# Kernel tuning notes

Measured on AMD Instinct MI355X. Metric: run time of the kernel, lower is better.

Reference implementation:

```python
import jax, jax.numpy as jnp
import numpy as np
from jax import lax

NB, HH, WW, C = 8, 64, 64, 192
G, K, DW_K, PA_K = 12, 3, 5, 3
GC, P = C // G, K * K
PAD, STRIDE, DIL = 1, 1, 1
OFFSET_SCALE = 1.0
LN_EPS = 1e-5


def _grid_sample(img, grid):
    # img: (B,Cc,H,W); grid: (B,L,P,2) xy in [-1,1]; bilinear, zeros padding, align_corners=False
    B, Cc, H, W = img.shape
    gx = (grid[..., 0] + 1.0) * (W * 0.5) - 0.5
    gy = (grid[..., 1] + 1.0) * (H * 0.5) - 0.5
    x0, y0 = jnp.floor(gx), jnp.floor(gy)

    def gather(xi, yi):
        valid = (xi >= 0) & (xi <= W - 1) & (yi >= 0) & (yi <= H - 1)
        xc = jnp.clip(xi, 0, W - 1).astype(jnp.int32)
        yc = jnp.clip(yi, 0, H - 1).astype(jnp.int32)
        v = jax.vmap(lambda im, y, x: im[:, y, x])(img, yc, xc)  # (B,Cc,L,P)
        return v * valid[:, None].astype(img.dtype)

    wx1, wy1 = gx - x0, gy - y0
    wx0, wy0 = 1.0 - wx1, 1.0 - wy1
    return (gather(x0, y0) * (wx0 * wy0)[:, None]
            + gather(x0 + 1.0, y0) * (wx1 * wy0)[:, None]
            + gather(x0, y0 + 1.0) * (wx0 * wy1)[:, None]
            + gather(x0 + 1.0, y0 + 1.0) * (wx1 * wy1)[:, None])


def _dcnv3_core(x, offset, mask):
    # x: (N,H,W,C) projected input; offset: (N,H,W,G*P*2); mask: (N,H,W,G*P)
    N, H, W, _ = x.shape
    xp = jnp.pad(x, ((0, 0), (PAD, PAD), (PAD, PAD), (0, 0)))
    Hp, Wp = H + 2 * PAD, W + 2 * PAD
    Ho, Wo = offset.shape[1], offset.shape[2]
    base = (DIL * (K - 1)) // 2 + 0.5
    ref_y = (base + jnp.arange(Ho) * STRIDE) / Hp
    ref_x = (base + jnp.arange(Wo) * STRIDE) / Wp
    ref = jnp.stack(jnp.broadcast_arrays(ref_x[None, :], ref_y[:, None]), -1)  # (Ho,Wo,2) xy
    start = -((DIL * (K - 1)) // 2)
    pts = (start + jnp.arange(K) * DIL).astype(x.dtype)
    gxg = jnp.broadcast_to((pts / Wp)[:, None], (K, K))  # w offset varies along dim0 (torch order)
    gyg = jnp.broadcast_to((pts / Hp)[None, :], (K, K))
    grid = jnp.tile(jnp.stack([gxg, gyg], -1).reshape(P, 2), (G, 1))  # (G*P,2)
    loc = ref[None, :, :, None, :] + grid * OFFSET_SCALE  # (1,Ho,Wo,G*P,2)
    norm = jnp.array([Wp, Hp], dtype=x.dtype)
    loc = loc + offset.reshape(N, Ho, Wo, G * P, 2) * OFFSET_SCALE / norm
    sg = 2.0 * loc - 1.0  # (N,Ho,Wo,G*P,2)
    img = xp.reshape(N, Hp * Wp, G, GC).transpose(0, 2, 3, 1).reshape(N * G, GC, Hp, Wp)
    grd = sg.reshape(N, Ho * Wo, G, P, 2).transpose(0, 2, 1, 3, 4).reshape(N * G, Ho * Wo, P, 2)
    samp = _grid_sample(img, grd)  # (N*G, GC, L, P)
    m = mask.reshape(N, Ho * Wo, G, P).transpose(0, 2, 1, 3).reshape(N * G, 1, Ho * Wo, P)
    out = (samp * m).sum(-1)  # (N*G, GC, L)
    return out.reshape(N, G, GC, Ho * Wo).transpose(0, 3, 1, 2).reshape(N, Ho, Wo, C)


def _dcnv3(x, dw_w, dw_b, ln_g, ln_b, off_w, off_b, msk_w, msk_b, in_w, in_b, out_w, out_b, cfs_w, cfs_b):
    N, H, W, _ = x.shape
    x_proj = x @ in_w + in_b
    # depthwise conv (5x5) -> LayerNorm (channels_last) -> GELU(exact)
    u = lax.conv_general_dilated(x, dw_w, (1, 1), 'SAME',
                                 dimension_numbers=('NHWC', 'HWIO', 'NHWC'),
                                 feature_group_count=C) + dw_b
    mu = u.mean(-1, keepdims=True)
    var = ((u - mu) ** 2).mean(-1, keepdims=True)
    u = (u - mu) * lax.rsqrt(var + LN_EPS) * ln_g + ln_b
    u = jax.nn.gelu(u, approximate=False)
    offset = u @ off_w + off_b  # (N,H,W,G*P*2)
    m = jax.nn.softmax((u @ msk_w + msk_b).reshape(N, H, W, G, P), axis=-1).reshape(N, H, W, G * P)
    y = _dcnv3_core(x_proj, offset, m)
    cfs = jax.nn.sigmoid(u @ cfs_w + cfs_b)  # (N,H,W,G)
    cfs = jnp.repeat(cfs, GC, axis=-1)       # (N,H,W,C), group-blockwise
    y = y * (1.0 - cfs) + x_proj * cfs
    return y @ out_w + out_b


def _patch_attention(x):
    # x: (N,H,W,C) -> std over softmax'd 3x3 neighbor scores: (N,H,W)
    N, H, W, _ = x.shape
    pad = (PA_K - 1) // 2
    xp = jnp.pad(x, ((0, 0), (pad, pad), (pad, pad), (0, 0)))
    neigh = jnp.stack([xp[:, i:i + H, j:j + W, :] for i in range(PA_K) for j in range(PA_K)],
                      axis=-1)  # (N,H,W,C,K1*K2), torch unfold ordering
    scores = jnp.einsum('nhwc,nhwck->nhwk', x, neigh)
    sm = jax.nn.softmax(scores, axis=-1)
    return jnp.std(sm, axis=-1, ddof=1)  # torch.std is unbiased


def setup_inputs() -> dict:
    key = jax.random.key(0)
    ks = jax.random.split(key, 8)
    s = 0.02
    return {
        'x': jax.random.normal(ks[0], (NB, HH, WW, C), jnp.float32),
        'dw_w': jax.random.normal(ks[1], (DW_K, DW_K, 1, C), jnp.float32) * s,
        'dw_b': jnp.zeros((C,), jnp.float32),
        'ln_g': jnp.ones((C,), jnp.float32),
        'ln_b': jnp.zeros((C,), jnp.float32),
        'off_w': jax.random.normal(ks[2], (C, G * P * 2), jnp.float32) * s,
        'off_b': jnp.zeros((G * P * 2,), jnp.float32),
        'msk_w': jax.random.normal(ks[3], (C, G * P), jnp.float32) * s,
        'msk_b': jnp.zeros((G * P,), jnp.float32),
        'in_w': jax.random.normal(ks[4], (C, C), jnp.float32) * s,
        'in_b': jnp.zeros((C,), jnp.float32),
        'out_w': jax.random.normal(ks[5], (C, C), jnp.float32) * s,
        'out_b': jnp.zeros((C,), jnp.float32),
        'cfs_w': jax.random.normal(ks[6], (C, G), jnp.float32) * s,
        'cfs_b': jnp.zeros((G,), jnp.float32),
    }


def reference(x, dw_w, dw_b, ln_g, ln_b, off_w, off_b, msk_w, msk_b, in_w, in_b, out_w, out_b, cfs_w, cfs_b):
    x1 = _dcnv3(x, dw_w, dw_b, ln_g, ln_b, off_w, off_b, msk_w, msk_b, in_w, in_b, out_w, out_b, cfs_w, cfs_b)
    mask = _patch_attention(x1)           # (N,H,W)
    return x + x1 * mask[..., None]
```

## Files before the change

### kernel.cpp

```cpp
#include <hip/hip_runtime.h>
#include <hip/hip_bf16.h>
#include <math.h>

#define NB 8
#define HH 64
#define WW 64
#define C 192
#define G 12
#define GC 16
#define P 9
#define NPIX (NB*HH*WW)

typedef __attribute__((ext_vector_type(8))) short short8;
typedef __attribute__((ext_vector_type(4))) float f32x4;
typedef unsigned short ushort;

__device__ __forceinline__ ushort to_bf16(float f) {
  __hip_bfloat16 b = __float2bfloat16(f);
  return *(ushort*)&b;
}
__device__ __forceinline__ float bf2f(ushort u) {
  union { unsigned u; float f; } cv; cv.u = ((unsigned)u) << 16; return cv.f;
}
__device__ __forceinline__ float bflo(unsigned u) {
  union { unsigned v; float f; } c; c.v = u << 16; return c.f;
}
__device__ __forceinline__ float bfhi(unsigned u) {
  union { unsigned v; float f; } c; c.v = u & 0xffff0000u; return c.f;
}

__global__ void prep_w_kernel(const float* __restrict__ in_w, const float* __restrict__ out_w,
    const float* __restrict__ off_w, const float* __restrict__ msk_w, const float* __restrict__ cfs_w,
    const float* __restrict__ off_b, const float* __restrict__ msk_b, const float* __restrict__ cfs_b,
    ushort* __restrict__ in_wt, ushort* __restrict__ out_wt, ushort* __restrict__ wf_t,
    float* __restrict__ bf_bias) {
  int idx = blockIdx.x*256 + threadIdx.x;
  if (idx < 36864) {
    int n = idx/192, k = idx%192;
    in_wt[idx] = to_bf16(in_w[k*192 + n]);
  } else if (idx < 73728) {
    int j = idx - 36864; int n = j/192, k = j%192;
    out_wt[j] = to_bf16(out_w[k*192 + n]);
  } else if (idx < 147456) {
    int j = idx - 73728; int n = j/192, k = j%192;
    float v = 0.f;
    if (n < 216)      v = off_w[k*216 + n];
    else if (n < 324) v = msk_w[k*108 + (n-216)];
    else if (n < 336) v = cfs_w[k*12  + (n-324)];
    wf_t[j] = to_bf16(v);
  }
  if (idx < 384) {
    float b = 0.f;
    if (idx < 216)      b = off_b[idx];
    else if (idx < 324) b = msk_b[idx-216];
    else if (idx < 336) b = cfs_b[idx-324];
    bf_bias[idx] = b;
  }
}

template<int NW, int NSTORE, bool BF16OUT, bool AF32>
__global__ __launch_bounds__(256) void mfma_gemm(const void* __restrict__ A_,
    const ushort* __restrict__ Wt, const float* __restrict__ bias,
    void* __restrict__ Cout_) {
  __shared__ ushort As[4*64*8];
  __shared__ ushort Bs[4*64*8];
  int pix0 = blockIdx.x * 64, n0 = blockIdx.y * 64;
  int tid = threadIdx.x;
  int wid = tid >> 6, lane = tid & 63;
  int wr = wid >> 1, wc = wid & 1;
  int lr = lane >> 4, lc = lane & 15;

  f32x4 acc[2][2];
  #pragma unroll
  for (int m=0;m<2;m++)
    #pragma unroll
    for (int j=0;j<2;j++) acc[m][j] = (f32x4){0.f,0.f,0.f,0.f};

  int s_kb = tid >> 6, s_row = tid & 63;

  short8 pa, pb;
  auto load_tile = [&](int k0) {
    if (AF32) {
      const float* Af = (const float*)A_;
      float4 u0 = *(const float4*)&Af[(size_t)(pix0 + s_row)*192 + k0 + s_kb*8];
      float4 u1 = *(const float4*)&Af[(size_t)(pix0 + s_row)*192 + k0 + s_kb*8 + 4];
      pa[0]=to_bf16(u0.x); pa[1]=to_bf16(u0.y); pa[2]=to_bf16(u0.z); pa[3]=to_bf16(u0.w);
      pa[4]=to_bf16(u1.x); pa[5]=to_bf16(u1.y); pa[6]=to_bf16(u1.z); pa[7]=to_bf16(u1.w);
    } else {
      const ushort* Ab = (const ushort*)A_;
      pa = *(const short8*)&Ab[(size_t)(pix0 + s_row)*192 + k0 + s_kb*8];
    }
    pb = *(const short8*)&Wt[(size_t)(n0 + s_row)*192 + k0 + s_kb*8];
  };
  load_tile(0);

  for (int t = 0; t < 6; t++) {
    __syncthreads();
    *(short8*)&As[(size_t)tid*8] = pa;
    *(short8*)&Bs[(size_t)tid*8] = pb;
    __syncthreads();
    if (t < 5) load_tile((t+1)*32);
    short8 a0 = *(const short8*)&As[(size_t)(lr*64 + wr*32 + lc)*8];
    short8 a1 = *(const short8*)&As[(size_t)(lr*64 + wr*32 + 16 + lc)*8];
    short8 b0 = *(const short8*)&Bs[(size_t)(lr*64 + wc*32 + lc)*8];
    short8 b1 = *(const short8*)&Bs[(size_t)(lr*64 + wc*32 + 16 + lc)*8];
    acc[0][0] = __builtin_amdgcn_mfma_f32_16x16x32_bf16(a0, b0, acc[0][0], 0,0,0);
    acc[0][1] = __builtin_amdgcn_mfma_f32_16x16x32_bf16(a0, b1, acc[0][1], 0,0,0);
    acc[1][0] = __builtin_amdgcn_mfma_f32_16x16x32_bf16(a1, b0, acc[1][0], 0,0,0);
    acc[1][1] = __builtin_amdgcn_mfma_f32_16x16x32_bf16(a1, b1, acc[1][1], 0,0,0);
  }
  #pragma unroll
  for (int j=0;j<2;j++) {
    int col = n0 + wc*32 + j*16 + lc;
    if (NW != NSTORE && col >= NSTORE) continue;
    float bb = bias[col];
    #pragma unroll
    for (int m=0;m<2;m++) {
      size_t rbase = pix0 + wr*32 + m*16 + lr*4;
      #pragma unroll
      for (int r=0;r<4;r++) {
        float v = acc[m][j][r] + bb;
        if (BF16OUT) ((ushort*)Cout_)[(rbase + r)*NSTORE + col] = to_bf16(v);
        else         ((float*) Cout_)[(rbase + r)*NSTORE + col] = v;
      }
    }
  }
}

#define SEG 16
__global__ __launch_bounds__(192) void dw_ln_gelu_kernel(const float* __restrict__ x,
    const float* __restrict__ dw_w, const float* __restrict__ dw_b,
    const float* __restrict__ ln_g, const float* __restrict__ ln_b,
    ushort* __restrict__ u_out) {
  int bid = blockIdx.x;
  int blk = (bid & 7) * 256 + (bid >> 3);
  int qw = blk & 3; int nh = blk >> 2;
  int h = nh & 63, n = nh >> 6;
  int c = threadIdx.x;
  int w0 = qw * SEG;

  float kw[25];
  #pragma unroll
  for (int t=0;t<25;t++) kw[t] = dw_w[t*C + c];

  float acc[SEG];
  float bb = dw_b[c];
  #pragma unroll
  for (int i=0;i<SEG;i++) acc[i] = bb;

  #pragma unroll
  for (int i=0;i<5;i++) {
    int hy = h + i - 2;
    if (hy < 0 || hy >= HH) continue;
    const float* rowp = &x[(((size_t)n*HH + hy)*WW)*C + c];
    #pragma unroll
    for (int wi=0; wi<SEG+4; wi++) {
      int w_in = w0 - 2 + wi;
      if (w_in < 0 || w_in >= WW) continue;
      float v = rowp[(size_t)w_in*C];
      #pragma unroll
      for (int j=0;j<5;j++) {
        int a = wi - j;
        if (a >= 0 && a < SEG) acc[a] += v * kw[i*5+j];
      }
    }
  }

  __shared__ float lds_acc[SEG][C+1];
  __shared__ float part1[SEG][12], part2[SEG][12];
  __shared__ float mu_s[SEG], rs_s[SEG];
  #pragma unroll
  for (int i=0;i<SEG;i++) lds_acc[i][c] = acc[i];
  __syncthreads();
  {
    int p = threadIdx.x & 15, chunk = threadIdx.x >> 4;
    float s1 = 0.f, s2 = 0.f;
    #pragma unroll
    for (int k=0;k<16;k++) {
      float v = lds_acc[p][chunk*16 + k];
      s1 += v; s2 += v*v;
    }
    part1[p][chunk] = s1; part2[p][chunk] = s2;
  }
  __syncthreads();
  if (threadIdx.x < SEG) {
    int p = threadIdx.x;
    float t1 = 0.f, t2 = 0.f;
    #pragma unroll
    for (int k=0;k<12;k++){ t1 += part1[p][k]; t2 += part2[p][k]; }
    float mu = t1 * (1.0f/C);
    float var = t2 * (1.0f/C) - mu*mu;
    mu_s[p] = mu; rs_s[p] = rsqrtf(var + 1e-5f);
  }
  __syncthreads();
  float gg = ln_g[c], lb = ln_b[c];
  size_t obase = ((size_t)nh*WW + w0)*C + c;
  #pragma unroll
  for (int i=0;i<SEG;i++) {
    float uv = (acc[i] - mu_s[i])*rs_s[i]*gg + lb;
    uv = 0.5f*uv*(1.0f + erff(uv*0.70710678118654752f));
    u_out[obase + (size_t)i*C] = to_bf16(uv);
  }
}

__global__ __launch_bounds__(256) void smprep_kernel(const ushort* __restrict__ omc,
    ushort* __restrict__ msm_pre, float* __restrict__ cfss) {
  int idx = blockIdx.x*256 + threadIdx.x;
  int px = idx / 12, g = idx % 12;
  const ushort* mrow = &omc[(size_t)px*336 + 216 + g*9];
  float lv[P];
  #pragma unroll
  for (int p=0;p<P;p++) lv[p] = bf2f(mrow[p]);
  float m = lv[0];
  #pragma unroll
  for (int p=1;p<P;p++) m = fmaxf(m, lv[p]);
  float s = 0.f;
  #pragma unroll
  for (int p=0;p<P;p++){ lv[p] = expf(lv[p]-m); s += lv[p]; }
  float cf = 1.0f/(1.0f+expf(-bf2f(omc[(size_t)px*336 + 324 + g])));
  cfss[idx] = cf;
  float onem = (1.0f - cf) / s;
  #pragma unroll
  for (int p=0;p<P;p++)
    msm_pre[(size_t)px*108 + g*9 + p] = to_bf16(lv[p]*onem);
}

__device__ __forceinline__ void fma8(float* acc, float w, uint4 q) {
  acc[0] += w*bflo(q.x); acc[1] += w*bfhi(q.x);
  acc[2] += w*bflo(q.y); acc[3] += w*bfhi(q.y);
  acc[4] += w*bflo(q.z); acc[5] += w*bfhi(q.z);
  acc[6] += w*bflo(q.w); acc[7] += w*bfhi(q.w);
}
__global__ __launch_bounds__(256) void gather_kernel(const ushort* __restrict__ omc,
    const ushort* __restrict__ msm_pre, const float* __restrict__ cfss,
    const ushort* __restrict__ x_proj, ushort* __restrict__ y_out) {
  int idx = blockIdx.x*256 + threadIdx.x;
  int px = idx / 24, s = idx - (idx/24)*24;
  int g = s >> 1;
  int n = px >> 12; int hw = px & 4095; int h = hw >> 6; int w = hw & 63;
  int cb = s * 16;
  const char* xb = (const char*)x_proj;
  const unsigned* omc32 = (const unsigned*)omc;
  int base = n*HH*WW*C;
  const float pts[3] = {-1.f, 0.f, 1.f};
  float acc[8] = {0.f,0.f,0.f,0.f,0.f,0.f,0.f,0.f};
  #pragma unroll
  for (int p=0;p<P;p++){
    unsigned off2 = omc32[(size_t)px*168 + g*9 + p];
    float ox = bflo(off2), oy = bfhi(off2);
    float gx = 1.0f + (float)w + pts[p/3] + ox;
    float gy = 1.0f + (float)h + pts[p%3] + oy;
    float x0f = floorf(gx), y0f = floorf(gy);
    float wx1 = gx - x0f, wy1 = gy - y0f;
    float wx0 = 1.f-wx1, wy0 = 1.f-wy1;
    int x0 = (int)x0f, y0 = (int)y0f;
    bool xv0 = (x0 >= 1) && (x0 <= 64);
    bool xv1 = (x0 >= 0) && (x0 <= 63);
    bool yv0 = (y0 >= 1) && (y0 <= 64);
    bool yv1 = (y0 >= 0) && (y0 <= 63);
    float m = bf2f(msm_pre[(size_t)px*108 + g*9 + p]);
    int a00 = (yv0&&xv0) ? (base + ((y0-1)*WW + (x0-1))*C)*2 : 0;
    int a01 = (yv0&&xv1) ? (base + ((y0-1)*WW + (x0  ))*C)*2 : 0;
    int a10 = (yv1&&xv0) ? (base + ((y0  )*WW + (x0-1))*C)*2 : 0;
    int a11 = (yv1&&xv1) ? (base + ((y0  )*WW + (x0  ))*C)*2 : 0;
    float w00 = (yv0&&xv0) ? wx0*wy0*m : 0.f;
    float w01 = (yv0&&xv1) ? wx1*wy0*m : 0.f;
    float w10 = (yv1&&xv0) ? wx0*wy1*m : 0.f;
    float w11 = (yv1&&xv1) ? wx1*wy1*m : 0.f;
    uint4 t0 = *(const uint4*)(xb + (unsigned)(a00 + cb));
    uint4 t1 = *(const uint4*)(xb + (unsigned)(a01 + cb));
    uint4 t2 = *(const uint4*)(xb + (unsigned)(a10 + cb));
    uint4 t3 = *(const uint4*)(xb + (unsigned)(a11 + cb));
    fma8(acc, w00, t0); fma8(acc, w01, t1);
    fma8(acc, w10, t2); fma8(acc, w11, t3);
  }
  float cf = cfss[px*12 + g];
  uint4 qx = *(const uint4*)(xb + ((size_t)px*C)*2 + cb);
  fma8(acc, cf, qx);
  short8 r;
  #pragma unroll
  for (int k=0;k<8;k++) r[k] = to_bf16(acc[k]);
  *(short8*)&y_out[(size_t)px*C + s*8] = r;
}

__global__ __launch_bounds__(256) void pattn_kernel(const float* __restrict__ x,
    const ushort* __restrict__ x1, float* __restrict__ out) {
  __shared__ unsigned xs[100*97];
  __shared__ float psc[64][36];
  __shared__ float sd_s[64];
  int blk = blockIdx.x;
  int n = blk >> 6;
  int ty = (blk >> 3) & 7, tx = blk & 7;
  int th0 = ty*8, tw0 = tx*8;
  int tid = threadIdx.x;
  const unsigned* x1u = (const unsigned*)x1;
  for (int i = tid; i < 100*96; i += 256) {
    int cell = i / 96, wd = i - cell*96;
    int gy = th0 - 1 + cell/10, gx = tw0 - 1 + cell%10;
    unsigned v = 0;
    if (gy>=0 && gy<HH && gx>=0 && gx<WW)
      v = x1u[(((size_t)n*HH+gy)*WW+gx)*96 + wd];
    xs[cell*97 + wd] = v;
  }
  __syncthreads();
  {
    int px = tid >> 2, qq = tid & 3;
    int py = px >> 3, pxx = px & 7;
    int cell = (py+1)*10 + (pxx+1);
    float cen[48];
    #pragma unroll
    for (int k=0;k<24;k++) {
      unsigned w = xs[cell*97 + qq*24 + k];
      cen[2*k] = bflo(w); cen[2*k+1] = bfhi(w);
    }
    #pragma unroll
    for (int ni=0;ni<9;ni++) {
      int nc = cell + (ni/3-1)*10 + (ni%3-1);
      float a = 0.f;
      #pragma unroll
      for (int k=0;k<24;k++) {
        unsigned w = xs[nc*97 + qq*24 + k];
        a += cen[2*k]*bflo(w) + cen[2*k+1]*bfhi(w);
      }
      psc[px][qq*9+ni] = a;
    }
  }
  __syncthreads();
  if (tid < 64) {
    float sc[9];
    #pragma unroll
    for (int k=0;k<9;k++)
      sc[k] = psc[tid][k] + psc[tid][9+k] + psc[tid][18+k] + psc[tid][27+k];
    float m = sc[0];
    #pragma unroll
    for (int k=1;k<9;k++) m = fmaxf(m, sc[k]);
    float pr[9]; float s = 0.f;
    #pragma unroll
    for (int k=0;k<9;k++){ pr[k] = expf(sc[k]-m); s += pr[k]; }
    float inv = 1.0f/s;
    float mean = 0.f;
    #pragma unroll
    for (int k=0;k<9;k++){ pr[k] *= inv; mean += pr[k]; }
    mean *= (1.0f/9.0f);
    float var = 0.f;
    #pragma unroll
    for (int k=0;k<9;k++){ float d = pr[k]-mean; var += d*d; }
    sd_s[tid] = sqrtf(var*(1.0f/8.0f));
  }
  __syncthreads();
  for (int i = tid; i < 64*96; i += 256) {
    int p2 = i / 96, wd = i - p2*96;
    int py2 = p2 >> 3, px2 = p2 & 7;
    unsigned v = xs[((py2+1)*10 + (px2+1))*97 + wd];
    size_t pix = ((size_t)n*HH + th0+py2)*WW + tw0+px2;
    float2 xv = ((const float2*)x)[pix*96 + wd];
    float sd = sd_s[p2];
    float2 o; o.x = xv.x + bflo(v)*sd; o.y = xv.y + bfhi(v)*sd;
    ((float2*)out)[pix*96 + wd] = o;
  }
}

extern "C" void kernel_launch(void* const* d_in, const int* in_sizes, int n_in,
                              void* d_out, int out_size, void* d_ws, size_t ws_size,
                              hipStream_t stream) {
  const float* x     = (const float*)d_in[0];
  const float* dw_w  = (const float*)d_in[1];
  const float* dw_b  = (const float*)d_in[2];
  const float* ln_g  = (const float*)d_in[3];
  const float* ln_b  = (const float*)d_in[4];
  const float* off_w = (const float*)d_in[5];
  const float* off_b = (const float*)d_in[6];
  const float* msk_w = (const float*)d_in[7];
  const float* msk_b = (const float*)d_in[8];
  const float* in_w  = (const float*)d_in[9];
  const float* in_b  = (const float*)d_in[10];
  const float* out_w = (const float*)d_in[11];
  const float* out_b = (const float*)d_in[12];
  const float* cfs_w = (const float*)d_in[13];
  const float* cfs_b = (const float*)d_in[14];
  float* outp = (float*)d_out;

  ushort* omc     = (ushort*)d_ws;
  ushort* xproj   = omc + (size_t)NPIX*336;
  ushort* x1_bf   = xproj + (size_t)NPIX*192;
  ushort* u_bf    = x1_bf + (size_t)NPIX*192;
  ushort* msm_pre = u_bf + (size_t)NPIX*192;
  float*  cfss    = (float*)(msm_pre + (size_t)NPIX*108);
  ushort* in_wt   = (ushort*)(cfss + (size_t)NPIX*12);
  ushort* out_wt  = in_wt + 192*192;
  ushort* wf_t    = out_wt + 192*192;
  float*  bfb     = (float*)(wf_t + 384*192);

  prep_w_kernel<<<(147456+255)/256, 256, 0, stream>>>(in_w, out_w, off_w, msk_w, cfs_w,
                                                       off_b, msk_b, cfs_b,
                                                       in_wt, out_wt, wf_t, bfb);
  mfma_gemm<192,192,true,true><<<dim3(NPIX/64, 3), 256, 0, stream>>>(x, in_wt, in_b, xproj);
  dw_ln_gelu_kernel<<<NB*HH*4, 192, 0, stream>>>(x, dw_w, dw_b, ln_g, ln_b, u_bf);
  mfma_gemm<384,336,true,false><<<dim3(NPIX/64, 6), 256, 0, stream>>>(u_bf, wf_t, bfb, omc);
  smprep_kernel<<<NPIX*12/256, 256, 0, stream>>>(omc, msm_pre, cfss);
  gather_kernel<<<NPIX*24/256, 256, 0, stream>>>(omc, msm_pre, cfss, xproj, u_bf);
  mfma_gemm<192,192,true,false><<<dim3(NPIX/64, 3), 256, 0, stream>>>(u_bf, out_wt, out_b, x1_bf);
  pattn_kernel<<<NB*64, 256, 0, stream>>>(x, x1_bf, outp);
}
```

Measured before the change: 158.1 us.

## Fuse softmax prep, deformable gather and output projection GEMM into one kernel

Three kernels (mask softmax/cfs sigmoid prep, bilinear deformable gather, and the output-projection MFMA GEMM) are merged into one kernel that handles one 64-pixel row per block. Intermediates (softmax mask, cfs, gathered y) stay in LDS instead of round-tripping through global memory, and the gather issues 12 loads at a time for more memory-level parallelism. Blocks are remapped to interleave images. The cost is heavy LDS use per block (about 40KB), which limits occupancy. The GEMM now runs on only 512 blocks, reading B straight from global memory with no LDS tiling.

```diff
diff --git a/kernel.cpp b/kernel.cpp
--- a/kernel.cpp
+++ b/kernel.cpp
@@ -203,84 +203,156 @@
   }
 }
 
-__global__ __launch_bounds__(256) void smprep_kernel(const ushort* __restrict__ omc,
-    ushort* __restrict__ msm_pre, float* __restrict__ cfss) {
-  int idx = blockIdx.x*256 + threadIdx.x;
-  int px = idx / 12, g = idx % 12;
-  const ushort* mrow = &omc[(size_t)px*336 + 216 + g*9];
-  float lv[P];
-  #pragma unroll
-  for (int p=0;p<P;p++) lv[p] = bf2f(mrow[p]);
-  float m = lv[0];
-  #pragma unroll
-  for (int p=1;p<P;p++) m = fmaxf(m, lv[p]);
-  float s = 0.f;
-  #pragma unroll
-  for (int p=0;p<P;p++){ lv[p] = expf(lv[p]-m); s += lv[p]; }
-  float cf = 1.0f/(1.0f+expf(-bf2f(omc[(size_t)px*336 + 324 + g])));
-  cfss[idx] = cf;
-  float onem = (1.0f - cf) / s;
-  #pragma unroll
-  for (int p=0;p<P;p++)
-    msm_pre[(size_t)px*108 + g*9 + p] = to_bf16(lv[p]*onem);
-}
-
+#define Y2STR 200
 __device__ __forceinline__ void fma8(float* acc, float w, uint4 q) {
   acc[0] += w*bflo(q.x); acc[1] += w*bfhi(q.x);
   acc[2] += w*bflo(q.y); acc[3] += w*bfhi(q.y);
   acc[4] += w*bflo(q.z); acc[5] += w*bfhi(q.z);
   acc[6] += w*bflo(q.w); acc[7] += w*bfhi(q.w);
 }
-__global__ __launch_bounds__(256) void gather_kernel(const ushort* __restrict__ omc,
-    const ushort* __restrict__ msm_pre, const float* __restrict__ cfss,
-    const ushort* __restrict__ x_proj, ushort* __restrict__ y_out) {
-  int idx = blockIdx.x*256 + threadIdx.x;
-  int px = idx / 24, s = idx - (idx/24)*24;
-  int g = s >> 1;
-  int n = px >> 12; int hw = px & 4095; int h = hw >> 6; int w = hw & 63;
-  int cb = s * 16;
-  const char* xb = (const char*)x_proj;
-  const unsigned* omc32 = (const unsigned*)omc;
-  int base = n*HH*WW*C;
-  const float pts[3] = {-1.f, 0.f, 1.f};
-  float acc[8] = {0.f,0.f,0.f,0.f,0.f,0.f,0.f,0.f};
-  #pragma unroll
-  for (int p=0;p<P;p++){
-    unsigned off2 = omc32[(size_t)px*168 + g*9 + p];
-    float ox = bflo(off2), oy = bfhi(off2);
-    float gx = 1.0f + (float)w + pts[p/3] + ox;
-    float gy = 1.0f + (float)h + pts[p%3] + oy;
-    float x0f = floorf(gx), y0f = floorf(gy);
-    float wx1 = gx - x0f, wy1 = gy - y0f;
-    float wx0 = 1.f-wx1, wy0 = 1.f-wy1;
-    int x0 = (int)x0f, y0 = (int)y0f;
-    bool xv0 = (x0 >= 1) && (x0 <= 64);
-    bool xv1 = (x0 >= 0) && (x0 <= 63);
-    bool yv0 = (y0 >= 1) && (y0 <= 64);
-    bool yv1 = (y0 >= 0) && (y0 <= 63);
-    float m = bf2f(msm_pre[(size_t)px*108 + g*9 + p]);
-    int a00 = (yv0&&xv0) ? (base + ((y0-1)*WW + (x0-1))*C)*2 : 0;
-    int a01 = (yv0&&xv1) ? (base + ((y0-1)*WW + (x0  ))*C)*2 : 0;
-    int a10 = (yv1&&xv0) ? (base + ((y0  )*WW + (x0-1))*C)*2 : 0;
-    int a11 = (yv1&&xv1) ? (base + ((y0  )*WW + (x0  ))*C)*2 : 0;
-    float w00 = (yv0&&xv0) ? wx0*wy0*m : 0.f;
-    float w01 = (yv0&&xv1) ? wx1*wy0*m : 0.f;
-    float w10 = (yv1&&xv0) ? wx0*wy1*m : 0.f;
-    float w11 = (yv1&&xv1) ? wx1*wy1*m : 0.f;
-    uint4 t0 = *(const uint4*)(xb + (unsigned)(a00 + cb));
-    uint4 t1 = *(const uint4*)(xb + (unsigned)(a01 + cb));
-    uint4 t2 = *(const uint4*)(xb + (unsigned)(a10 + cb));
-    uint4 t3 = *(const uint4*)(xb + (unsigned)(a11 + cb));
-    fma8(acc, w00, t0); fma8(acc, w01, t1);
-    fma8(acc, w10, t2); fma8(acc, w11, t3);
-  }
-  float cf = cfss[px*12 + g];
-  uint4 qx = *(const uint4*)(xb + ((size_t)px*C)*2 + cb);
-  fma8(acc, cf, qx);
-  short8 r;
-  #pragma unroll
-  for (int k=0;k<8;k++) r[k] = to_bf16(acc[k]);
-  *(short8*)&y_out[(size_t)px*C + s*8] = r;
+__global__ __launch_bounds__(256) void samgemm_kernel(const ushort* __restrict__ omc,
+    const ushort* __restrict__ x_proj, const ushort* __restrict__ out_wt,
+    const float* __restrict__ out_b, ushort* __restrict__ x1_out) {
+  __shared__ ushort y2lds[64*Y2STR];
+  __shared__ ushort msm_lds[64*108];
+  __shared__ float  cfs_lds[64*12];
+  int bid = blockIdx.x;
+  int blk = (bid & 7) * 64 + (bid >> 3);
+  int pix0 = blk * 64;
+  int n = pix0 >> 12; int h = (pix0 & 4095) >> 6;
+  int tid = threadIdx.x;
+
+  #pragma unroll
+  for (int k = 0; k < 3; k++) {
+    int task = tid + k*256;
+    int pxl = task / 12, g = task % 12;
+    size_t pix = pix0 + pxl;
+    const ushort* mrow = &omc[pix*336 + 216 + g*9];
+    float lv[P];
+    #pragma unroll
+    for (int p=0;p<P;p++) lv[p] = bf2f(mrow[p]);
+    float m = lv[0];
+    #pragma unroll
+    for (int p=1;p<P;p++) m = fmaxf(m, lv[p]);
+    float s = 0.f;
+    #pragma unroll
+    for (int p=0;p<P;p++){ lv[p] = expf(lv[p]-m); s += lv[p]; }
+    float cf = 1.0f/(1.0f+expf(-bf2f(omc[pix*336 + 324 + g])));
+    cfs_lds[task] = cf;
+    float onem = (1.0f - cf) / s;
+    #pragma unroll
+    for (int p=0;p<P;p++)
+      msm_lds[pxl*108 + g*9 + p] = to_bf16(lv[p]*onem);
+  }
+  __syncthreads();
+
+  {
+    const char* xb = (const char*)x_proj;
+    const unsigned* omc32 = (const unsigned*)omc;
+    int base = n*HH*WW*C;
+    const float pts[3] = {-1.f, 0.f, 1.f};
+    #pragma unroll
+    for (int k = 0; k < 6; k++) {
+      int task = tid + k*256;
+      int pxl = task / 24, s = task - (task/24)*24;
+      int g = s >> 1;
+      int w = pxl;
+      size_t pix = pix0 + pxl;
+      int cb = s * 16;
+      float acc[8] = {0.f,0.f,0.f,0.f,0.f,0.f,0.f,0.f};
+      #pragma unroll
+      for (int pb = 0; pb < 3; pb++) {
+        int a_[12]; float w_[12];
+        #pragma unroll
+        for (int j3 = 0; j3 < 3; j3++) {
+          int p = pb*3 + j3;
+          unsigned off2 = omc32[pix*168 + g*9 + p];
+          float ox = bflo(off2), oy = bfhi(off2);
+          float gx = 1.0f + (float)w + pts[p/3] + ox;
+          float gy = 1.0f + (float)h + pts[p%3] + oy;
+          float x0f = floorf(gx), y0f = floorf(gy);
+          float wx1 = gx-x0f, wy1 = gy-y0f;
+          float wx0 = 1.f-wx1, wy0 = 1.f-wy1;
+          int x0 = (int)x0f, y0 = (int)y0f;
+          bool xv0 = (x0>=1)&&(x0<=64), xv1 = (x0>=0)&&(x0<=63);
+          bool yv0 = (y0>=1)&&(y0<=64), yv1 = (y0>=0)&&(y0<=63);
+          float m = bf2f(msm_lds[pxl*108 + g*9 + p]);
+          a_[j3*4+0] = (yv0&&xv0) ? (base + ((y0-1)*WW + (x0-1))*C)*2 : 0;
+          a_[j3*4+1] = (yv0&&xv1) ? (base + ((y0-1)*WW + (x0  ))*C)*2 : 0;
+          a_[j3*4+2] = (yv1&&xv0) ? (base + ((y0  )*WW + (x0-1))*C)*2 : 0;
+          a_[j3*4+3] = (yv1&&xv1) ? (base + ((y0  )*WW + (x0  ))*C)*2 : 0;
+          w_[j3*4+0] = (yv0&&xv0) ? wx0*wy0*m : 0.f;
+          w_[j3*4+1] = (yv0&&xv1) ? wx1*wy0*m : 0.f;
+          w_[j3*4+2] = (yv1&&xv0) ? wx0*wy1*m : 0.f;
+          w_[j3*4+3] = (yv1&&xv1) ? wx1*wy1*m : 0.f;
+        }
+        uint4 t0 = *(const uint4*)(xb + (unsigned)(a_[0] + cb));
+        uint4 t1 = *(const uint4*)(xb + (unsigned)(a_[1] + cb));
+        uint4 t2 = *(const uint4*)(xb + (unsigned)(a_[2] + cb));
+        uint4 t3 = *(const uint4*)(xb + (unsigned)(a_[3] + cb));
+        uint4 t4 = *(const uint4*)(xb + (unsigned)(a_[4] + cb));
+        uint4 t5 = *(const uint4*)(xb + (unsigned)(a_[5] + cb));
+        uint4 t6 = *(const uint4*)(xb + (unsigned)(a_[6] + cb));
+        uint4 t7 = *(const uint4*)(xb + (unsigned)(a_[7] + cb));
+        uint4 t8 = *(const uint4*)(xb + (unsigned)(a_[8] + cb));
+        uint4 t9 = *(const uint4*)(xb + (unsigned)(a_[9] + cb));
+        uint4 ta = *(const uint4*)(xb + (unsigned)(a_[10] + cb));
+        uint4 tb = *(const uint4*)(xb + (unsigned)(a_[11] + cb));
+        fma8(acc, w_[0], t0); fma8(acc, w_[1], t1);
+        fma8(acc, w_[2], t2); fma8(acc, w_[3], t3);
+        fma8(acc, w_[4], t4); fma8(acc, w_[5], t5);
+        fma8(acc, w_[6], t6); fma8(acc, w_[7], t7);
+        fma8(acc, w_[8], t8); fma8(acc, w_[9], t9);
+        fma8(acc, w_[10], ta); fma8(acc, w_[11], tb);
+      }
+      float cf = cfs_lds[pxl*12 + g];
+      uint4 qx = *(const uint4*)(xb + pix*384 + cb);
+      fma8(acc, cf, qx);
+      short8 r;
+      #pragma unroll
+      for (int q=0;q<8;q++) r[q] = to_bf16(acc[q]);
+      *(short8*)&y2lds[pxl*Y2STR + s*8] = r;
+    }
+  }
+  __syncthreads();
+
+  {
+    int wid = tid >> 6, lane = tid & 63;
+    int wr = wid >> 1, wc = wid & 1;
+    int lr = lane >> 4, lc = lane & 15;
+    #pragma unroll
+    for (int n0t = 0; n0t < 3; n0t++) {
+      int n0 = n0t * 64;
+      f32x4 acc[2][2];
+      #pragma unroll
+      for (int m=0;m<2;m++)
+        #pragma unroll
+        for (int j=0;j<2;j++) acc[m][j] = (f32x4){0.f,0.f,0.f,0.f};
+      #pragma unroll
+      for (int t = 0; t < 6; t++) {
+        short8 a0 = *(const short8*)&y2lds[(wr*32 + lc)*Y2STR + t*32 + lr*8];
+        short8 a1 = *(const short8*)&y2lds[(wr*32 + 16 + lc)*Y2STR + t*32 + lr*8];
+        short8 b0 = *(const short8*)&out_wt[(size_t)(n0 + wc*32 + lc)*192 + t*32 + lr*8];
+        short8 b1 = *(const short8*)&out_wt[(size_t)(n0 + wc*32 + 16 + lc)*192 + t*32 + lr*8];
+        acc[0][0] = __builtin_amdgcn_mfma_f32_16x16x32_bf16(a0, b0, acc[0][0], 0,0,0);
+        acc[0][1] = __builtin_amdgcn_mfma_f32_16x16x32_bf16(a0, b1, acc[0][1], 0,0,0);
+        acc[1][0] = __builtin_amdgcn_mfma_f32_16x16x32_bf16(a1, b0, acc[1][0], 0,0,0);
+        acc[1][1] = __builtin_amdgcn_mfma_f32_16x16x32_bf16(a1, b1, acc[1][1], 0,0,0);
+      }
+      #pragma unroll
+      for (int j=0;j<2;j++) {
+        int col = n0 + wc*32 + j*16 + lc;
+        float bb = out_b[col];
+        #pragma unroll
+        for (int m=0;m<2;m++) {
+          size_t rbase = pix0 + wr*32 + m*16 + lr*4;
+          #pragma unroll
+          for (int r=0;r<4;r++)
+            x1_out[(rbase + r)*192 + col] = to_bf16(acc[m][j][r] + bb);
+        }
+      }
+    }
+  }
 }
 
 __global__ __launch_bounds__(256) void pattn_kernel(const float* __restrict__ x,
@@ -384,9 +456,7 @@
   ushort* xproj   = omc + (size_t)NPIX*336;
   ushort* x1_bf   = xproj + (size_t)NPIX*192;
   ushort* u_bf    = x1_bf + (size_t)NPIX*192;
-  ushort* msm_pre = u_bf + (size_t)NPIX*192;
-  float*  cfss    = (float*)(msm_pre + (size_t)NPIX*108);
-  ushort* in_wt   = (ushort*)(cfss + (size_t)NPIX*12);
+  ushort* in_wt   = u_bf + (size_t)NPIX*192;
   ushort* out_wt  = in_wt + 192*192;
   ushort* wf_t    = out_wt + 192*192;
   float*  bfb     = (float*)(wf_t + 384*192);
@@ -397,8 +467,6 @@
   mfma_gemm<192,192,true,true><<<dim3(NPIX/64, 3), 256, 0, stream>>>(x, in_wt, in_b, xproj);
   dw_ln_gelu_kernel<<<NB*HH*4, 192, 0, stream>>>(x, dw_w, dw_b, ln_g, ln_b, u_bf);
   mfma_gemm<384,336,true,false><<<dim3(NPIX/64, 6), 256, 0, stream>>>(u_bf, wf_t, bfb, omc);
-  smprep_kernel<<<NPIX*12/256, 256, 0, stream>>>(omc, msm_pre, cfss);
-  gather_kernel<<<NPIX*24/256, 256, 0, stream>>>(omc, msm_pre, cfss, xproj, u_bf);
-  mfma_gemm<192,192,true,false><<<dim3(NPIX/64, 3), 256, 0, stream>>>(u_bf, out_wt, out_b, x1_bf);
+  samgemm_kernel<<<NPIX/64, 256, 0, stream>>>(omc, xproj, out_wt, out_b, x1_bf);
   pattn_kernel<<<NB*64, 256, 0, stream>>>(x, x1_bf, outp);
 }
```

New measurement: 178.7 us. 13.1% more time.
